# Kernel tuning notes

Measured on AMD Instinct MI355X. Metric: run time of the kernel, lower is better.

The kernel has to match this reference:

```python
import jax, jax.numpy as jnp
import numpy as np


def conv2d(x, w, b, pad=0):
    y = jax.lax.conv_general_dilated(x, w, (1, 1), [(pad, pad), (pad, pad)],
                                     dimension_numbers=('NCHW', 'OIHW', 'NCHW'))
    return y + b[None, :, None, None]


def leaky(x):
    return jnp.where(x >= 0, x, 0.1 * x)


def adaptive_pool3(x):
    # exact AdaptiveAvgPool2d((3,3)) when H,W divisible by 3
    B, C, H, W = x.shape
    return x.reshape(B, C, 3, H // 3, 3, W // 3).mean(axis=(3, 5))


def psf2otf(ker, H, W):
    # circularly shift PSF so its centre is at (0,0), then FFT (DWDN convention)
    B, C, kh, kw = ker.shape
    c = kh // 2 + 1
    psf = jnp.zeros((B, C, H, W), ker.dtype)
    psf = psf.at[:, :, :c, :c].set(ker[:, :, c - 1:, c - 1:])
    psf = psf.at[:, :, :c, -(c - 1):].set(ker[:, :, c - 1:, :c - 1])
    psf = psf.at[:, :, -(c - 1):, :c].set(ker[:, :, :c - 1, c - 1:])
    psf = psf.at[:, :, -(c - 1):, -(c - 1):].set(ker[:, :, :c - 1, :c - 1])
    return jnp.fft.fft2(psf)


def setup_inputs() -> dict:
    key = jax.random.key(0)
    ks = jax.random.split(key, 16)
    B, NF, C, H = 8, 64, 16, 246
    x = jax.random.normal(ks[0], (B, NF, H, H), jnp.float32)
    kernel = jax.random.uniform(ks[1], (B, 1, 21, 21), jnp.float32)
    kernel = kernel / kernel.sum(axis=(2, 3), keepdims=True)  # normalized blur PSF
    def w(k, shape):
        fan_in = shape[1] * shape[2] * shape[3]
        return jax.random.normal(k, shape, jnp.float32) / np.sqrt(fan_in)
    return {
        'x': x, 'kernel': kernel,
        'w_red': w(ks[2], (C, NF, 1, 1)), 'b_red': jnp.zeros((C,), jnp.float32),
        'w_g1': w(ks[3], (C, C, 3, 3)), 'b_g1': jnp.zeros((C,), jnp.float32),
        'w_g2': w(ks[4], (C, C, 3, 3)), 'b_g2': jnp.zeros((C,), jnp.float32),
        'w_g3': w(ks[5], (C, C, 3, 3)), 'b_g3': jnp.zeros((C,), jnp.float32),
        'w_g4': w(ks[6], (C, C, 1, 1)), 'b_g4': jnp.zeros((C,), jnp.float32),
        'w_exp': w(ks[7], (NF, C, 1, 1)), 'b_exp': jnp.zeros((NF,), jnp.float32),
    }


def reference(x, kernel, w_red, b_red, w_g1, b_g1, w_g2, b_g2, w_g3, b_g3,
              w_g4, b_g4, w_exp, b_exp):
    cls_feats = conv2d(x, w_red, b_red)                      # [B,C,H,W]
    h = leaky(conv2d(cls_feats, w_g1, b_g1))                 # valid 3x3 convs
    h = leaky(conv2d(h, w_g2, b_g2))
    h = conv2d(h, w_g3, b_g3)
    h = adaptive_pool3(h)                                    # [B,C,3,3]
    kernel_P = jnp.exp(conv2d(h, w_g4, b_g4))
    kernel_P = kernel_P - kernel_P.mean(axis=(2, 3), keepdims=True)

    ks_ = kernel.shape[-1]
    fp = jnp.pad(cls_feats, ((0, 0), (0, 0), (ks_, ks_), (ks_, ks_)), mode='edge')
    Hp, Wp = fp.shape[2], fp.shape[3]
    # batched Wiener deconvolution over all channels at once (replaces per-channel loop)
    Kf = psf2otf(kernel, Hp, Wp)                             # [B,1,Hp,Wp] complex
    Pf = psf2otf(kernel_P, Hp, Wp)                           # [B,C,Hp,Wp] complex
    denom = Kf.real ** 2 + Kf.imag ** 2 + Pf.real ** 2 + Pf.imag ** 2
    inv_ker = jnp.conj(Kf) / denom                           # conj(K)/(|K|^2+|P|^2)
    deblur = jnp.fft.ifft2(inv_ker * jnp.fft.fft2(fp)).real
    clear = deblur[:, :, ks_:-ks_, ks_:-ks_]
    return conv2d(clear, w_exp, b_exp)
```

## Files before the change

kernel.cpp:

```cpp
#include <hip/hip_runtime.h>
#include <hip/hip_bf16.h>

__device__ inline float2 cadd(float2 a, float2 b){ return make_float2(a.x+b.x, a.y+b.y); }
__device__ inline float2 csub(float2 a, float2 b){ return make_float2(a.x-b.x, a.y-b.y); }
__device__ inline float2 cmul(float2 a, float2 b){
    return make_float2(fmaf(a.x,b.x,-a.y*b.y), fmaf(a.x,b.y,a.y*b.x));
}

#define NPIX 60516
#define NFFT 288
#define NFFT2 82944
#define XW 152
#define SPLANE (NFFT*XW)

__device__ inline int lidx(int i, int c){ return i*8 + (i>>2) + c; }
#define LDSN 2376

template<bool INV>
__device__ inline void bf4(float2 a0, float2 a1, float2 a2, float2 a3,
                           float2& b0, float2& b1, float2& b2, float2& b3) {
    float2 t0=cadd(a0,a2), t1=csub(a0,a2), t2=cadd(a1,a3), t3=csub(a1,a3);
    b0=cadd(t0,t2); b2=csub(t0,t2);
    if (!INV) { b1=make_float2(t1.x+t3.y, t1.y-t3.x); b3=make_float2(t1.x-t3.y, t1.y+t3.x); }
    else      { b1=make_float2(t1.x-t3.y, t1.y+t3.x); b3=make_float2(t1.x+t3.y, t1.y-t3.x); }
}
template<bool INV>
__device__ inline void bf3(float2 a0, float2 a1, float2 a2,
                           float2& b0, float2& b1, float2& b2) {
    const float d = INV ? 0.8660254037844386f : -0.8660254037844386f;
    float2 tt=cadd(a1,a2), u=csub(a1,a2);
    b0=cadd(a0,tt);
    b1=make_float2(a0.x-0.5f*tt.x - d*u.y, a0.y-0.5f*tt.y + d*u.x);
    b2=make_float2(a0.x-0.5f*tt.x + d*u.y, a0.y-0.5f*tt.y - d*u.x);
}

template<bool INV>
__device__ inline void fft288_row(float2*& X, float2*& Y, int lane, const float2* __restrict__ tw) {
    auto TW = [&](int k) { float2 v = tw[k]; if (INV) v.y = -v.y; return v; };
    for (int p = lane; p < 72; p += 64) {
        float2 b0,b1,b2,b3;
        bf4<INV>(X[p], X[p+72], X[p+144], X[p+216], b0,b1,b2,b3);
        Y[4*p]=b0; Y[4*p+1]=cmul(b1,TW(p)); Y[4*p+2]=cmul(b2,TW(2*p)); Y[4*p+3]=cmul(b3,TW(3*p));
    }
    __syncthreads(); { float2* t=X; X=Y; Y=t; }
    for (int it = lane; it < 72; it += 64) {
        int p = it>>2, q = it&3, i0 = q+4*p;
        float2 b0,b1,b2,b3;
        bf4<INV>(X[i0], X[i0+72], X[i0+144], X[i0+216], b0,b1,b2,b3);
        int o = q+16*p;
        Y[o]=b0; Y[o+4]=cmul(b1,TW(4*p)); Y[o+8]=cmul(b2,TW(8*p)); Y[o+12]=cmul(b3,TW(12*p));
    }
    __syncthreads(); { float2* t=X; X=Y; Y=t; }
    for (int it = lane; it < 144; it += 64) {
        int p = it>>4, q = it&15, i0 = q+16*p;
        float2 a0=X[i0], a1=X[i0+144];
        int o = q+32*p;
        Y[o]=cadd(a0,a1); Y[o+16]=cmul(csub(a0,a1),TW(16*p));
    }
    __syncthreads(); { float2* t=X; X=Y; Y=t; }
    for (int it = lane; it < 96; it += 64) {
        int p = it>>5, q = it&31, i0 = q+32*p;
        float2 b0,b1,b2;
        bf3<INV>(X[i0], X[i0+96], X[i0+192], b0,b1,b2);
        int o = q+96*p;
        Y[o]=b0; Y[o+32]=cmul(b1,TW(32*p)); Y[o+64]=cmul(b2,TW(64*p));
    }
    __syncthreads(); { float2* t=X; X=Y; Y=t; }
    for (int q = lane; q < 96; q += 64) {
        float2 b0,b1,b2;
        bf3<INV>(X[q], X[q+96], X[q+192], b0,b1,b2);
        Y[q]=b0; Y[q+96]=b1; Y[q+192]=b2;
    }
    __syncthreads(); { float2* t=X; X=Y; Y=t; }
}

template<bool INV>
__device__ inline void fft288_s9(float2*& X, float2*& Y, int w, int c, const float2* __restrict__ tw) {
    auto TW = [&](int k) { float2 v = tw[k]; if (INV) v.y = -v.y; return v; };
    for (int p = w; p < 72; p += 32) {
        float2 b0,b1,b2,b3;
        bf4<INV>(X[lidx(p,c)], X[lidx(p+72,c)], X[lidx(p+144,c)], X[lidx(p+216,c)], b0,b1,b2,b3);
        Y[lidx(4*p,c)]=b0; Y[lidx(4*p+1,c)]=cmul(b1,TW(p));
        Y[lidx(4*p+2,c)]=cmul(b2,TW(2*p)); Y[lidx(4*p+3,c)]=cmul(b3,TW(3*p));
    }
    __syncthreads(); { float2* t=X; X=Y; Y=t; }
    for (int it = w; it < 72; it += 32) {
        int p = it>>2, q = it&3, i0 = q+4*p;
        float2 b0,b1,b2,b3;
        bf4<INV>(X[lidx(i0,c)], X[lidx(i0+72,c)], X[lidx(i0+144,c)], X[lidx(i0+216,c)], b0,b1,b2,b3);
        int o = q+16*p;
        Y[lidx(o,c)]=b0; Y[lidx(o+4,c)]=cmul(b1,TW(4*p));
        Y[lidx(o+8,c)]=cmul(b2,TW(8*p)); Y[lidx(o+12,c)]=cmul(b3,TW(12*p));
    }
    __syncthreads(); { float2* t=X; X=Y; Y=t; }
    for (int it = w; it < 144; it += 32) {
        int p = it>>4, q = it&15, i0 = q+16*p;
        float2 a0=X[lidx(i0,c)], a1=X[lidx(i0+144,c)];
        int o = q+32*p;
        Y[lidx(o,c)]=cadd(a0,a1); Y[lidx(o+16,c)]=cmul(csub(a0,a1),TW(16*p));
    }
    __syncthreads(); { float2* t=X; X=Y; Y=t; }
    for (int it = w; it < 96; it += 32) {
        int p = it>>5, q = it&31, i0 = q+32*p;
        float2 b0,b1,b2;
        bf3<INV>(X[lidx(i0,c)], X[lidx(i0+96,c)], X[lidx(i0+192,c)], b0,b1,b2);
        int o = q+96*p;
        Y[lidx(o,c)]=b0; Y[lidx(o+32,c)]=cmul(b1,TW(32*p)); Y[lidx(o+64,c)]=cmul(b2,TW(64*p));
    }
    __syncthreads(); { float2* t=X; X=Y; Y=t; }
    for (int q = w; q < 96; q += 32) {
        float2 b0,b1,b2;
        bf3<INV>(X[lidx(q,c)], X[lidx(q+96,c)], X[lidx(q+192,c)], b0,b1,b2);
        Y[lidx(q,c)]=b0; Y[lidx(q+96,c)]=b1; Y[lidx(q+192,c)]=b2;
    }
    __syncthreads(); { float2* t=X; X=Y; Y=t; }
}

__global__ void k_tw(float2* tw, float* pooled) {
    int t = threadIdx.x;
    if (t < NFFT) {
        double ang = -2.0 * 3.14159265358979323846 * (double)t / (double)NFFT;
        tw[t] = make_float2((float)cos(ang), (float)sin(ang));
    }
    for (int i = t; i < 1152; i += 320) pooled[i] = 0.f;
}

__global__ __launch_bounds__(256) void k_conv1x1_red(const float* __restrict__ x,
        const float* __restrict__ w, const float* __restrict__ bias, float* __restrict__ out) {
    const int NP4 = NPIX/4;
    int idx = blockIdx.x * 256 + threadIdx.x;
    if (idx >= 8 * NP4) return;
    int b = idx / NP4, p4 = idx % NP4;
    const float4* xb = (const float4*)(x + (size_t)b * 64 * NPIX) + p4;
    float4 acc[16];
    #pragma unroll
    for (int co = 0; co < 16; co++) { float bb = bias[co]; acc[co] = make_float4(bb,bb,bb,bb); }
    for (int ci = 0; ci < 64; ci++) {
        float4 v = xb[(size_t)ci * NP4];
        #pragma unroll
        for (int co = 0; co < 16; co++) {
            float wv = w[co*64+ci];
            acc[co].x = fmaf(wv, v.x, acc[co].x);
            acc[co].y = fmaf(wv, v.y, acc[co].y);
            acc[co].z = fmaf(wv, v.z, acc[co].z);
            acc[co].w = fmaf(wv, v.w, acc[co].w);
        }
    }
    float4* ob = (float4*)(out + (size_t)b * 16 * NPIX) + p4;
    #pragma unroll
    for (int co = 0; co < 16; co++) ob[(size_t)co*NP4] = acc[co];
}

template<int HIN, bool LEAKY>
__global__ __launch_bounds__(256) void k_conv3x3(const float* __restrict__ in,
        const float* __restrict__ w, const float* __restrict__ bias, float* __restrict__ out) {
    const int HOUT = HIN - 2;
    const int GX = (HOUT + 3) / 4;
    int idx = blockIdx.x * 256 + threadIdx.x;
    if (idx >= 8 * HOUT * GX) return;
    int b  = idx / (HOUT * GX);
    int r  = idx % (HOUT * GX);
    int oy = r / GX;
    int ox0 = (r % GX) * 4;

    float acc[16][4];
    #pragma unroll
    for (int co = 0; co < 16; co++) {
        float bb = bias[co];
        #pragma unroll
        for (int px = 0; px < 4; px++) acc[co][px] = bb;
    }
    const float* ib = in + (size_t)b * 16 * HIN * HIN + (size_t)oy * HIN;
    for (int ci = 0; ci < 16; ci++) {
        const float* ic = ib + (size_t)ci * HIN * HIN;
        #pragma unroll
        for (int ky = 0; ky < 3; ky++) {
            float in6[6];
            #pragma unroll
            for (int j = 0; j < 6; j++) {
                int xx = ox0 + j;
                if (HOUT % 4 != 0) { if (xx > HIN - 1) xx = HIN - 1; }
                in6[j] = ic[ky * HIN + xx];
            }
            #pragma unroll
            for (int kx = 0; kx < 3; kx++) {
                #pragma unroll
                for (int co = 0; co < 16; co++) {
                    float wv = w[co*144 + ci*9 + ky*3 + kx];
                    #pragma unroll
                    for (int px = 0; px < 4; px++)
                        acc[co][px] = fmaf(wv, in6[px + kx], acc[co][px]);
                }
            }
        }
    }
    float* ob = out + (size_t)b * 16 * HOUT * HOUT + (size_t)oy * HOUT + ox0;
    #pragma unroll
    for (int co = 0; co < 16; co++) {
        #pragma unroll
        for (int px = 0; px < 4; px++) {
            if (HOUT % 4 == 0 || ox0 + px < HOUT) {
                float v = acc[co][px];
                if (LEAKY) v = (v >= 0.f) ? v : 0.1f * v;
                ob[(size_t)co * HOUT * HOUT + px] = v;
            }
        }
    }
}

__global__ __launch_bounds__(256) void k_conv3x3_pool(const float* __restrict__ in,
        const float* __restrict__ w, const float* __restrict__ bias, float* __restrict__ pooled) {
    const int HIN = 242, GX = 60;
    __shared__ float cs[144];
    int t = threadIdx.x;
    int b = blockIdx.x / 57;
    int r = (blockIdx.x % 57) * 256 + t;
    bool valid = r < 14400;
    float partial[16];
    int cell = 0;
    if (valid) {
        int oy = r / GX, ox0 = (r % GX) * 4;
        cell = (oy / 80) * 3 + (ox0 / 80);
        float acc[16][4];
        #pragma unroll
        for (int co = 0; co < 16; co++) {
            float bb = bias[co];
            #pragma unroll
            for (int px = 0; px < 4; px++) acc[co][px] = bb;
        }
        const float* ib = in + (size_t)b * 16 * HIN * HIN + (size_t)oy * HIN;
        for (int ci = 0; ci < 16; ci++) {
            const float* ic = ib + (size_t)ci * HIN * HIN;
            #pragma unroll
            for (int ky = 0; ky < 3; ky++) {
                float in6[6];
                #pragma unroll
                for (int j = 0; j < 6; j++) in6[j] = ic[ky * HIN + ox0 + j];
                #pragma unroll
                for (int kx = 0; kx < 3; kx++) {
                    #pragma unroll
                    for (int co = 0; co < 16; co++) {
                        float wv = w[co*144 + ci*9 + ky*3 + kx];
                        #pragma unroll
                        for (int px = 0; px < 4; px++)
                            acc[co][px] = fmaf(wv, in6[px + kx], acc[co][px]);
                    }
                }
            }
        }
        #pragma unroll
        for (int co = 0; co < 16; co++)
            partial[co] = (acc[co][0] + acc[co][1]) + (acc[co][2] + acc[co][3]);
    }
    if (t < 144) cs[t] = 0.f;
    __syncthreads();
    if (valid) {
        #pragma unroll
        for (int co = 0; co < 16; co++) atomicAdd(&cs[co*9 + cell], partial[co]);
    }
    __syncthreads();
    if (t < 144) atomicAdd(&pooled[b*144 + t], cs[t]);
}

__global__ void k_kernelP(const float* __restrict__ pooled, const float* __restrict__ w,
                          const float* __restrict__ bias, float* __restrict__ out) {
    int b = blockIdx.x / 16, co = blockIdx.x % 16;
    __shared__ float vals[9];
    int t = threadIdx.x;
    if (t < 9) {
        float a = 0.f;
        for (int ci = 0; ci < 16; ci++) a += pooled[(b*16+ci)*9 + t] * w[co*16+ci];
        vals[t] = expf(bias[co] + a * (1.f/6400.f));
    }
    __syncthreads();
    if (t < 9) {
        float m = 0.f;
        #pragma unroll
        for (int i = 0; i < 9; i++) m += vals[i];
        m *= (1.f/9.f);
        out[(b*16+co)*9 + t] = vals[t] - m;
    }
}

__global__ __launch_bounds__(256) void k_psfKT(const float* __restrict__ ker, float2* __restrict__ KfT) {
    int idx = blockIdx.x*256 + threadIdx.x;
    if (idx >= 8*NFFT2) return;
    int pos = idx % NFFT2, b = idx / NFFT2;
    int u = pos / NFFT, v = pos % NFFT;
    int ry = (v < 11) ? v+10 : ((v >= 278) ? v-278 : -1);
    int rx = (u < 11) ? u+10 : ((u >= 278) ? u-278 : -1);
    float val = (ry >= 0 && rx >= 0) ? ker[b*441 + ry*21 + rx] : 0.f;
    KfT[idx] = make_float2(val, 0.f);
}

template<bool INV>
__global__ __launch_bounds__(256) void k_fft_rows(float2* __restrict__ M, const float2* __restrict__ tw) {
    __shared__ float2 A[4][NFFT];
    __shared__ float2 B[4][NFFT];
    int t = threadIdx.x, w = t >> 6, lane = t & 63;
    size_t row = (size_t)blockIdx.x*4 + w;
    float2* X = A[w]; float2* Y = B[w];
    float2* s = M + row*NFFT;
    for (int j = lane; j < NFFT; j += 64) X[j] = s[j];
    __syncthreads();
    fft288_row<INV>(X, Y, lane, tw);
    for (int j = lane; j < NFFT; j += 64) s[j] = X[j];
}

template<bool INV>
__global__ __launch_bounds__(256) void k_fft_cols(float2* __restrict__ M, const float2* __restrict__ tw) {
    __shared__ float2 Abuf[LDSN];
    __shared__ float2 Bbuf[LDSN];
    int t = threadIdx.x, c = t & 7, w = t >> 3;
    int ch = blockIdx.x / 36, cg = blockIdx.x % 36;
    float2* base = M + (size_t)ch * NFFT2 + cg*8 + c;
    float2* X = Abuf; float2* Y = Bbuf;
    for (int r = w; r < NFFT; r += 32) X[lidx(r,c)] = base[(size_t)r * NFFT];
    __syncthreads();
    fft288_s9<INV>(X, Y, w, c, tw);
    for (int r = w; r < NFFT; r += 32) base[(size_t)r * NFFT] = X[lidx(r,c)];
}

__global__ __launch_bounds__(256) void k_fft_rows_pad_half(const float* __restrict__ cls,
        float2* __restrict__ S, const float2* __restrict__ tw) {
    __shared__ float2 A[4][NFFT];
    __shared__ float2 B[4][NFFT];
    int t = threadIdx.x, w = t >> 6, lane = t & 63;
    size_t row = (size_t)blockIdx.x*4 + w;
    int pc = (int)(row / NFFT), y = (int)(row % NFFT);
    int iy = min(max(y-21, 0), 245);
    const float* c0 = cls + (size_t)(2*pc)*NPIX + (size_t)iy*246;
    float2* X = A[w]; float2* Y = B[w];
    for (int j = lane; j < NFFT; j += 64) {
        int ix = min(max(j-21, 0), 245);
        X[j] = make_float2(c0[ix], c0[NPIX+ix]);
    }
    __syncthreads();
    fft288_row<false>(X, Y, lane, tw);
    int chA = (pc >> 3)*16 + (pc & 7)*2;
    float2* sA = S + (size_t)chA * SPLANE + (size_t)y * XW;
    float2* sB = sA + SPLANE;
    for (int x = lane; x < XW; x += 64) {
        float2 Av = make_float2(0.f, 0.f), Bv = make_float2(0.f, 0.f);
        if (x <= 144) {
            int m = (NFFT - x) % NFFT;
            float2 zk = X[x], zm = X[m];
            Av = make_float2(0.5f*(zk.x+zm.x),  0.5f*(zk.y-zm.y));
            Bv = make_float2(0.5f*(zk.y+zm.y), -0.5f*(zk.x-zm.x));
        }
        sA[x] = Av; sB[x] = Bv;
    }
}

__global__ __launch_bounds__(256) void k_fft_cols_filter(float2* __restrict__ S,
        const float2* __restrict__ KfT, const float* __restrict__ kP, const float2* __restrict__ tw) {
    __shared__ float2 Abuf[LDSN];
    __shared__ float2 Bbuf[LDSN];
    int t = threadIdx.x, c = t & 7, w = t >> 3;
    int g = blockIdx.x / 128, ch = blockIdx.x % 128;
    int xg = g*8 + c;
    int b = ch >> 4;
    float2* sb = S + (size_t)ch * SPLANE + xg;
    float2* X = Abuf; float2* Y = Bbuf;
    for (int r = w; r < NFFT; r += 32) X[lidx(r,c)] = sb[(size_t)r * XW];
    __syncthreads();
    fft288_s9<false>(X, Y, w, c, tw);
    {
        const float* p9 = kP + ch*9;
        float2 wx = tw[xg];
        const float2* Kcol = KfT + (size_t)b*NFFT2 + (size_t)xg*NFFT;
        for (int y = w; y < NFFT; y += 32) {
            float2 v = X[lidx(y,c)];
            float2 K = Kcol[y];
            float2 wy = tw[y];
            float2 R0 = make_float2(p9[1] + (p9[0]+p9[2])*wx.x, (p9[2]-p9[0])*wx.y);
            float2 R1 = make_float2(p9[4] + (p9[3]+p9[5])*wx.x, (p9[5]-p9[3])*wx.y);
            float2 R2 = make_float2(p9[7] + (p9[6]+p9[8])*wx.x, (p9[8]-p9[6])*wx.y);
            float2 P;
            P.x = R1.x + wy.x*(R0.x+R2.x) - wy.y*(R2.y-R0.y);
            P.y = R1.y + wy.x*(R0.y+R2.y) + wy.y*(R2.x-R0.x);
            float kk = K.x*K.x + K.y*K.y;
            float rcp = 1.0f / (kk + P.x*P.x + P.y*P.y);
            float2 H = make_float2(K.x*rcp, -K.y*rcp);
            Y[lidx(y,c)] = cmul(H, v);
        }
    }
    __syncthreads();
    { float2* tp = X; X = Y; Y = tp; }
    fft288_s9<true>(X, Y, w, c, tw);
    for (int r = w; r < NFFT; r += 32)
        if (r >= 21 && r < 267) sb[(size_t)r * XW] = X[lidx(r,c)];
}

__global__ __launch_bounds__(256) void k_ifft_rows_conv(const float2* __restrict__ S,
        const float* __restrict__ w_exp, const float* __restrict__ b_exp,
        float* __restrict__ out, const float2* __restrict__ tw) {
    __shared__ float2 Abuf[LDSN];
    __shared__ float2 Bbuf[LDSN];
    int t = threadIdx.x, c = t & 7, w = t >> 3;
    int b = blockIdx.x / 246;
    int rseq = blockIdx.x % 246;
    int y = rseq + 21;
    int chA = b*16 + 2*c;
    const float2* sA = S + (size_t)chA * SPLANE + (size_t)y * XW;
    const float2* sB = sA + SPLANE;
    float2* X = Abuf; float2* Y = Bbuf;
    for (int j = w; j < NFFT; j += 32) {
        float2 z;
        if (j <= 144) {
            float2 a = sA[j], bb = sB[j];
            z = make_float2(a.x - bb.y, a.y + bb.x);
        } else {
            int m = NFFT - j;
            float2 a = sA[m], bb = sB[m];
            z = make_float2(a.x + bb.y, bb.x - a.y);
        }
        X[lidx(j,c)] = z;
    }
    __syncthreads();
    fft288_s9<true>(X, Y, w, c, tw);
    if (t < 246) {
        const float sc = 1.0f / 82944.0f;
        float v[16];
        #pragma unroll
        for (int h = 0; h < 8; h++) {
            float2 z = X[lidx(t + 21, h)];
            v[2*h]   = z.x * sc;
            v[2*h+1] = z.y * sc;
        }
        float* ob = out + (size_t)b * 64 * NPIX + (size_t)rseq * 246 + t;
        #pragma unroll
        for (int co = 0; co < 64; co++) {
            float a = b_exp[co];
            #pragma unroll
            for (int ci = 0; ci < 16; ci++) a = fmaf(w_exp[co*16+ci], v[ci], a);
            ob[(size_t)co * NPIX] = a;
        }
    }
}

extern "C" void kernel_launch(void* const* d_in, const int* in_sizes, int n_in,
                              void* d_out, int out_size, void* d_ws, size_t ws_size,
                              hipStream_t stream) {
    const float* x     = (const float*)d_in[0];
    const float* ker   = (const float*)d_in[1];
    const float* w_red = (const float*)d_in[2];
    const float* b_red = (const float*)d_in[3];
    const float* w_g1  = (const float*)d_in[4];
    const float* b_g1  = (const float*)d_in[5];
    const float* w_g2  = (const float*)d_in[6];
    const float* b_g2  = (const float*)d_in[7];
    const float* w_g3  = (const float*)d_in[8];
    const float* b_g3  = (const float*)d_in[9];
    const float* w_g4  = (const float*)d_in[10];
    const float* b_g4  = (const float*)d_in[11];
    const float* w_exp = (const float*)d_in[12];
    const float* b_exp = (const float*)d_in[13];
    float* out = (float*)d_out;

    char* ws = (char*)d_ws;
    size_t off = 0;
    auto alloc = [&](size_t bytes) -> char* {
        char* p = ws + off; off += (bytes + 255) & ~(size_t)255; return p;
    };
    float*  cls    = (float*) alloc(7746048ull * 4);
    float2* S      = (float2*)alloc((size_t)128 * SPLANE * 8);
    float*  hb     = (float*) alloc(7495712ull * 4);
    float2* KfT    = (float2*)alloc((size_t)8 * NFFT2 * 8);
    float*  pooled = (float*) alloc(1152 * 4);
    float*  kP     = (float*) alloc(1152 * 4);
    float2* tw     = (float2*)alloc(288 * 8);
    float*  ha     = (float*)S;

    k_tw<<<1, 320, 0, stream>>>(tw, pooled);
    k_conv1x1_red<<<473, 256, 0, stream>>>(x, w_red, b_red, cls);
    k_conv3x3<246, true ><<<466, 256, 0, stream>>>(cls, w_g1, b_g1, ha);
    k_conv3x3<244, true ><<<462, 256, 0, stream>>>(ha,  w_g2, b_g2, hb);
    k_conv3x3_pool<<<456, 256, 0, stream>>>(hb, w_g3, b_g3, pooled);
    k_kernelP<<<128, 64, 0, stream>>>(pooled, w_g4, b_g4, kP);

    k_psfKT<<<2592, 256, 0, stream>>>(ker, KfT);
    k_fft_rows<false><<<576, 256, 0, stream>>>(KfT, tw);
    k_fft_cols<false><<<288, 256, 0, stream>>>(KfT, tw);

    k_fft_rows_pad_half<<<4608, 256, 0, stream>>>(cls, S, tw);

    k_fft_cols_filter<<<19*128, 256, 0, stream>>>(S, KfT, kP, tw);

    k_ifft_rows_conv<<<1968, 256, 0, stream>>>(S, w_exp, b_exp, out, tw);
}
```

Measured before the change: 341.7 us.

## Assign each FFT column to a single wavefront and use wave barriers

Reassigns the shared-memory FFT work so that each column (or row) transform is handled by one 32/64-lane group inside a single wavefront. This lets the inter-stage block-wide __syncthreads be replaced by wave-level barriers. Block barriers are kept only around the global load and store phases, where threads touch columns owned by other waves. The aim is to cut block-wide synchronization stalls across the many FFT stages, at the cost of a changed thread-to-data mapping. That mapping depends on 32-lane groups sharing a 64-wide wavefront for correctness.

```diff
diff --git a/kernel.cpp b/kernel.cpp
--- a/kernel.cpp
+++ b/kernel.cpp
@@ -12,6 +12,8 @@
 #define NFFT2 82944
 #define XW 152
 #define SPLANE (NFFT*XW)
+
+#define WSYNC() do { __builtin_amdgcn_wave_barrier(); asm volatile("" ::: "memory"); } while (0)
 
 __device__ inline int lidx(int i, int c){ return i*8 + (i>>2) + c; }
 #define LDSN 2376
@@ -42,7 +44,7 @@
         bf4<INV>(X[p], X[p+72], X[p+144], X[p+216], b0,b1,b2,b3);
         Y[4*p]=b0; Y[4*p+1]=cmul(b1,TW(p)); Y[4*p+2]=cmul(b2,TW(2*p)); Y[4*p+3]=cmul(b3,TW(3*p));
     }
-    __syncthreads(); { float2* t=X; X=Y; Y=t; }
+    WSYNC(); { float2* t=X; X=Y; Y=t; }
     for (int it = lane; it < 72; it += 64) {
         int p = it>>2, q = it&3, i0 = q+4*p;
         float2 b0,b1,b2,b3;
@@ -50,14 +52,14 @@
         int o = q+16*p;
         Y[o]=b0; Y[o+4]=cmul(b1,TW(4*p)); Y[o+8]=cmul(b2,TW(8*p)); Y[o+12]=cmul(b3,TW(12*p));
     }
-    __syncthreads(); { float2* t=X; X=Y; Y=t; }
+    WSYNC(); { float2* t=X; X=Y; Y=t; }
     for (int it = lane; it < 144; it += 64) {
         int p = it>>4, q = it&15, i0 = q+16*p;
         float2 a0=X[i0], a1=X[i0+144];
         int o = q+32*p;
         Y[o]=cadd(a0,a1); Y[o+16]=cmul(csub(a0,a1),TW(16*p));
     }
-    __syncthreads(); { float2* t=X; X=Y; Y=t; }
+    WSYNC(); { float2* t=X; X=Y; Y=t; }
     for (int it = lane; it < 96; it += 64) {
         int p = it>>5, q = it&31, i0 = q+32*p;
         float2 b0,b1,b2;
@@ -65,13 +67,13 @@
         int o = q+96*p;
         Y[o]=b0; Y[o+32]=cmul(b1,TW(32*p)); Y[o+64]=cmul(b2,TW(64*p));
     }
-    __syncthreads(); { float2* t=X; X=Y; Y=t; }
+    WSYNC(); { float2* t=X; X=Y; Y=t; }
     for (int q = lane; q < 96; q += 64) {
         float2 b0,b1,b2;
         bf3<INV>(X[q], X[q+96], X[q+192], b0,b1,b2);
         Y[q]=b0; Y[q+96]=b1; Y[q+192]=b2;
     }
-    __syncthreads(); { float2* t=X; X=Y; Y=t; }
+    WSYNC(); { float2* t=X; X=Y; Y=t; }
 }
 
 template<bool INV>
@@ -83,7 +85,7 @@
         Y[lidx(4*p,c)]=b0; Y[lidx(4*p+1,c)]=cmul(b1,TW(p));
         Y[lidx(4*p+2,c)]=cmul(b2,TW(2*p)); Y[lidx(4*p+3,c)]=cmul(b3,TW(3*p));
     }
-    __syncthreads(); { float2* t=X; X=Y; Y=t; }
+    WSYNC(); { float2* t=X; X=Y; Y=t; }
     for (int it = w; it < 72; it += 32) {
         int p = it>>2, q = it&3, i0 = q+4*p;
         float2 b0,b1,b2,b3;
@@ -92,14 +94,14 @@
         Y[lidx(o,c)]=b0; Y[lidx(o+4,c)]=cmul(b1,TW(4*p));
         Y[lidx(o+8,c)]=cmul(b2,TW(8*p)); Y[lidx(o+12,c)]=cmul(b3,TW(12*p));
     }
-    __syncthreads(); { float2* t=X; X=Y; Y=t; }
+    WSYNC(); { float2* t=X; X=Y; Y=t; }
     for (int it = w; it < 144; it += 32) {
         int p = it>>4, q = it&15, i0 = q+16*p;
         float2 a0=X[lidx(i0,c)], a1=X[lidx(i0+144,c)];
         int o = q+32*p;
         Y[lidx(o,c)]=cadd(a0,a1); Y[lidx(o+16,c)]=cmul(csub(a0,a1),TW(16*p));
     }
-    __syncthreads(); { float2* t=X; X=Y; Y=t; }
+    WSYNC(); { float2* t=X; X=Y; Y=t; }
     for (int it = w; it < 96; it += 32) {
         int p = it>>5, q = it&31, i0 = q+32*p;
         float2 b0,b1,b2;
@@ -107,13 +109,13 @@
         int o = q+96*p;
         Y[lidx(o,c)]=b0; Y[lidx(o+32,c)]=cmul(b1,TW(32*p)); Y[lidx(o+64,c)]=cmul(b2,TW(64*p));
     }
-    __syncthreads(); { float2* t=X; X=Y; Y=t; }
+    WSYNC(); { float2* t=X; X=Y; Y=t; }
     for (int q = w; q < 96; q += 32) {
         float2 b0,b1,b2;
         bf3<INV>(X[lidx(q,c)], X[lidx(q+96,c)], X[lidx(q+192,c)], b0,b1,b2);
         Y[lidx(q,c)]=b0; Y[lidx(q+96,c)]=b1; Y[lidx(q+192,c)]=b2;
     }
-    __syncthreads(); { float2* t=X; X=Y; Y=t; }
+    WSYNC(); { float2* t=X; X=Y; Y=t; }
 }
 
 __global__ void k_tw(float2* tw, float* pooled) {
@@ -302,7 +304,7 @@
     float2* X = A[w]; float2* Y = B[w];
     float2* s = M + row*NFFT;
     for (int j = lane; j < NFFT; j += 64) X[j] = s[j];
-    __syncthreads();
+    WSYNC();
     fft288_row<INV>(X, Y, lane, tw);
     for (int j = lane; j < NFFT; j += 64) s[j] = X[j];
 }
@@ -312,12 +314,14 @@
     __shared__ float2 Abuf[LDSN];
     __shared__ float2 Bbuf[LDSN];
     int t = threadIdx.x, c = t & 7, w = t >> 3;
+    int f = t >> 5, l = t & 31;
     int ch = blockIdx.x / 36, cg = blockIdx.x % 36;
     float2* base = M + (size_t)ch * NFFT2 + cg*8 + c;
     float2* X = Abuf; float2* Y = Bbuf;
     for (int r = w; r < NFFT; r += 32) X[lidx(r,c)] = base[(size_t)r * NFFT];
     __syncthreads();
-    fft288_s9<INV>(X, Y, w, c, tw);
+    fft288_s9<INV>(X, Y, l, f, tw);
+    __syncthreads();
     for (int r = w; r < NFFT; r += 32) base[(size_t)r * NFFT] = X[lidx(r,c)];
 }
 
@@ -335,7 +339,7 @@
         int ix = min(max(j-21, 0), 245);
         X[j] = make_float2(c0[ix], c0[NPIX+ix]);
     }
-    __syncthreads();
+    WSYNC();
     fft288_row<false>(X, Y, lane, tw);
     int chA = (pc >> 3)*16 + (pc & 7)*2;
     float2* sA = S + (size_t)chA * SPLANE + (size_t)y * XW;
@@ -357,20 +361,21 @@
     __shared__ float2 Abuf[LDSN];
     __shared__ float2 Bbuf[LDSN];
     int t = threadIdx.x, c = t & 7, w = t >> 3;
+    int f = t >> 5, l = t & 31;
     int g = blockIdx.x / 128, ch = blockIdx.x % 128;
-    int xg = g*8 + c;
     int b = ch >> 4;
-    float2* sb = S + (size_t)ch * SPLANE + xg;
+    float2* sb = S + (size_t)ch * SPLANE + g*8;
     float2* X = Abuf; float2* Y = Bbuf;
-    for (int r = w; r < NFFT; r += 32) X[lidx(r,c)] = sb[(size_t)r * XW];
-    __syncthreads();
-    fft288_s9<false>(X, Y, w, c, tw);
+    for (int r = w; r < NFFT; r += 32) X[lidx(r,c)] = sb[(size_t)r * XW + c];
+    __syncthreads();
+    fft288_s9<false>(X, Y, l, f, tw);
     {
         const float* p9 = kP + ch*9;
-        float2 wx = tw[xg];
-        const float2* Kcol = KfT + (size_t)b*NFFT2 + (size_t)xg*NFFT;
-        for (int y = w; y < NFFT; y += 32) {
-            float2 v = X[lidx(y,c)];
+        int xgf = g*8 + f;
+        float2 wx = tw[xgf];
+        const float2* Kcol = KfT + (size_t)b*NFFT2 + (size_t)xgf*NFFT;
+        for (int y = l; y < NFFT; y += 32) {
+            float2 v = X[lidx(y,f)];
             float2 K = Kcol[y];
             float2 wy = tw[y];
             float2 R0 = make_float2(p9[1] + (p9[0]+p9[2])*wx.x, (p9[2]-p9[0])*wx.y);
@@ -382,14 +387,15 @@
             float kk = K.x*K.x + K.y*K.y;
             float rcp = 1.0f / (kk + P.x*P.x + P.y*P.y);
             float2 H = make_float2(K.x*rcp, -K.y*rcp);
-            Y[lidx(y,c)] = cmul(H, v);
-        }
-    }
-    __syncthreads();
+            Y[lidx(y,f)] = cmul(H, v);
+        }
+    }
+    WSYNC();
     { float2* tp = X; X = Y; Y = tp; }
-    fft288_s9<true>(X, Y, w, c, tw);
+    fft288_s9<true>(X, Y, l, f, tw);
+    __syncthreads();
     for (int r = w; r < NFFT; r += 32)
-        if (r >= 21 && r < 267) sb[(size_t)r * XW] = X[lidx(r,c)];
+        if (r >= 21 && r < 267) sb[(size_t)r * XW + c] = X[lidx(r,c)];
 }
 
 __global__ __launch_bounds__(256) void k_ifft_rows_conv(const float2* __restrict__ S,
@@ -397,15 +403,17 @@
         float* __restrict__ out, const float2* __restrict__ tw) {
     __shared__ float2 Abuf[LDSN];
     __shared__ float2 Bbuf[LDSN];
-    int t = threadIdx.x, c = t & 7, w = t >> 3;
+    int t = threadIdx.x;
+    int f = t >> 5, l = t & 31;
     int b = blockIdx.x / 246;
     int rseq = blockIdx.x % 246;
     int y = rseq + 21;
-    int chA = b*16 + 2*c;
-    const float2* sA = S + (size_t)chA * SPLANE + (size_t)y * XW;
-    const float2* sB = sA + SPLANE;
+    const float2* sbase = S + (size_t)(b*16) * SPLANE + (size_t)y * XW;
     float2* X = Abuf; float2* Y = Bbuf;
-    for (int j = w; j < NFFT; j += 32) {
+    for (int idx = t; idx < 2304; idx += 256) {
+        int h = idx & 7, j = idx >> 3;
+        const float2* sA = sbase + (size_t)(2*h) * SPLANE;
+        const float2* sB = sA + SPLANE;
         float2 z;
         if (j <= 144) {
             float2 a = sA[j], bb = sB[j];
@@ -415,10 +423,11 @@
             float2 a = sA[m], bb = sB[m];
             z = make_float2(a.x + bb.y, bb.x - a.y);
         }
-        X[lidx(j,c)] = z;
-    }
-    __syncthreads();
-    fft288_s9<true>(X, Y, w, c, tw);
+        X[lidx(j,h)] = z;
+    }
+    __syncthreads();
+    fft288_s9<true>(X, Y, l, f, tw);
+    __syncthreads();
     if (t < 246) {
         const float sc = 1.0f / 82944.0f;
         float v[16];
```

New measurement: 338.8 us. Within noise of the previous version (-0.8%).
